# Performance work log

Hardware: AMD Instinct MI355X
Metric: run time of the kernel (lower is better)

## Reference

```python
import jax, jax.numpy as jnp
import numpy as np

B, V, N, H, C_OUT = 16, 8192, 2048, 128, 7


def setup_inputs() -> dict:
    key = jax.random.key(0)
    ks = jax.random.split(key, 5)
    return {
        "verts": jax.random.normal(ks[0], (B, V, 3), jnp.float32) * 10.0,
        "coords_ca": jax.random.normal(ks[1], (B, N, 3), jnp.float32) * 10.0,
        "feats": jax.random.normal(ks[2], (B, N, H), jnp.float32),
        "W1": jax.random.normal(ks[3], (H, H), jnp.float32) / np.sqrt(H),
        "b1": jnp.zeros((H,), jnp.float32),
        "W2": jax.random.normal(ks[4], (H, C_OUT), jnp.float32) / np.sqrt(H),
        "b2": jnp.zeros((C_OUT,), jnp.float32),
    }


def reference(verts, coords_ca, feats, W1, b1, W2, b2):
    # Per-graph: nearest-CA match for every surface vertex (cdist + argmin),
    # then sum over the UNIQUE set of matched residues (torch: processed[min_indices.unique()].sum(-2)).
    # Equivalent jit-friendly form: hit-mask over residues, masked sum.
    def per_graph(v, c, f):
        # squared euclidean distances [V, N]; argmin is invariant to the sqrt
        d = (jnp.sum(v * v, -1)[:, None]
             - 2.0 * (v @ c.T)
             + jnp.sum(c * c, -1)[None, :])
        mi = jnp.argmin(d, axis=1)                       # [V] nearest residue per vertex
        hit = jnp.zeros((c.shape[0],), f.dtype).at[mi].add(1.0)
        mask = (hit > 0).astype(f.dtype)                 # [N] residue selected at least once
        return jnp.einsum('nh,n->h', f, mask)            # sum over unique selected residues

    pooled = jax.vmap(per_graph)(verts, coords_ca, feats)  # [B, H]
    # top_net (Dropout is identity in eval)
    h = jax.nn.relu(pooled @ W1 + b1)
    return h @ W2 + b2                                    # [B, 7]
```

## Files before the change

kernel.cpp:

```cpp
#include <hip/hip_runtime.h>
#include <hip/hip_bf16.h>

#define B_GR   16
#define V_PTS  8192
#define N_RES  2048
#define H_DIM  128
#define C_OUT  7
#define SEGS   16

#define NSPLIT 16
#define NL     (N_RES / NSPLIT)
#define VPT    8
#define VBLK   (256 * VPT)
#define VBLKS  (V_PTS / VBLK)

__global__ __launch_bounds__(256, 4) void k_argmin(const float* __restrict__ verts,
                                                   const float* __restrict__ coords,
                                                   unsigned long long* __restrict__ mi64) {
    __shared__ float4 sc[NL];
    const int b  = blockIdx.x / (VBLKS * NSPLIT);
    const int r  = blockIdx.x % (VBLKS * NSPLIT);
    const int vb = r / NSPLIT;
    const int ns = r % NSPLIT;

    const float* cbase = coords + ((size_t)b * N_RES + ns * NL) * 3;
    if (threadIdx.x < NL) {
        const int i = threadIdx.x;
        float x = cbase[i * 3 + 0];
        float y = cbase[i * 3 + 1];
        float z = cbase[i * 3 + 2];
        float csq = __fadd_rn(__fadd_rn(__fmul_rn(x, x), __fmul_rn(y, y)), __fmul_rn(z, z));
        sc[i] = make_float4(x, y, z, csq);
    }
    __syncthreads();

    const int vbase = vb * VBLK + threadIdx.x;
    const float* vp = verts + (size_t)b * V_PTS * 3;

    float vx[VPT], vy[VPT], vz[VPT], vsq[VPT], best[VPT];
    int bi[VPT];
#pragma unroll
    for (int k = 0; k < VPT; ++k) {
        const int v = vbase + k * 256;
        vx[k] = vp[v * 3 + 0];
        vy[k] = vp[v * 3 + 1];
        vz[k] = vp[v * 3 + 2];
        vsq[k] = __fadd_rn(__fadd_rn(__fmul_rn(vx[k], vx[k]), __fmul_rn(vy[k], vy[k])),
                           __fmul_rn(vz[k], vz[k]));
        best[k] = 3.402823466e+38f;
        bi[k] = 0;
    }

#pragma unroll 2
    for (int n = 0; n < NL; ++n) {
        const float4 c = sc[n];
#pragma unroll
        for (int k = 0; k < VPT; ++k) {
            float dot = __fadd_rn(__fadd_rn(__fmul_rn(vx[k], c.x), __fmul_rn(vy[k], c.y)),
                                  __fmul_rn(vz[k], c.z));
            float d = __fadd_rn(fmaf(-2.0f, dot, vsq[k]), c.w);
            bool m = d < best[k];
            best[k] = m ? d : best[k];
            bi[k]   = m ? n : bi[k];
        }
    }

#pragma unroll
    for (int k = 0; k < VPT; ++k) {
        unsigned int bits = __float_as_uint(best[k]);
        unsigned int key  = bits ^ (unsigned int)(((int)bits >> 31) | 0x80000000);
        unsigned long long packed =
            ((unsigned long long)key << 32) | (unsigned int)(ns * NL + bi[k]);
        atomicMin(&mi64[(size_t)b * V_PTS + vbase + k * 256], packed);
    }
}

__global__ __launch_bounds__(256) void k_pool(const unsigned long long* __restrict__ mi64,
                                              const float* __restrict__ feats,
                                              float* __restrict__ partial) {
    __shared__ float msk[N_RES];
    __shared__ float4 red[8][32];
    const int b   = blockIdx.x >> 4;
    const int seg = blockIdx.x & (SEGS - 1);

    for (int i = threadIdx.x; i < N_RES; i += 256) msk[i] = 0.0f;
    __syncthreads();

    const unsigned long long* mb = mi64 + (size_t)b * V_PTS;
    for (int v = threadIdx.x; v < V_PTS; v += 256)
        msk[(unsigned int)mb[v]] = 1.0f;
    __syncthreads();

    const int q = threadIdx.x & 31;
    const int s = threadIdx.x >> 5;
    const int n0 = seg * (N_RES / SEGS);
    const float4* fb4 = (const float4*)(feats + ((size_t)b * N_RES + n0) * H_DIM);

    float4 acc = make_float4(0.f, 0.f, 0.f, 0.f);
#pragma unroll
    for (int n = 0; n < N_RES / SEGS / 8; ++n) {
        const int nn = s + n * 8;
        const float m = msk[n0 + nn];
        const float4 f = fb4[(size_t)nn * 32 + q];
        acc.x = fmaf(f.x, m, acc.x);
        acc.y = fmaf(f.y, m, acc.y);
        acc.z = fmaf(f.z, m, acc.z);
        acc.w = fmaf(f.w, m, acc.w);
    }
    red[s][q] = acc;
    __syncthreads();

    if (s == 0) {
        float4 t = acc;
#pragma unroll
        for (int i = 1; i < 8; ++i) {
            t.x += red[i][q].x; t.y += red[i][q].y;
            t.z += red[i][q].z; t.w += red[i][q].w;
        }
        ((float4*)partial)[((size_t)b * SEGS + seg) * 32 + q] = t;
    }
}

__global__ __launch_bounds__(128) void k_mlp(const float* __restrict__ partial,
                                             const float* __restrict__ W1,
                                             const float* __restrict__ b1,
                                             const float* __restrict__ W2,
                                             const float* __restrict__ b2,
                                             float* __restrict__ out) {
    __shared__ float pooled[H_DIM];
    __shared__ float h1[H_DIM];
    const int b = blockIdx.x;
    const int j = threadIdx.x;

    float s = 0.0f;
#pragma unroll
    for (int g = 0; g < SEGS; ++g)
        s += partial[((size_t)b * SEGS + g) * H_DIM + j];
    pooled[j] = s;
    __syncthreads();

    float acc = b1[j];
#pragma unroll 8
    for (int hh = 0; hh < H_DIM; ++hh)
        acc = fmaf(pooled[hh], W1[hh * H_DIM + j], acc);
    h1[j] = fmaxf(acc, 0.0f);
    __syncthreads();

    if (j < C_OUT) {
        float o = b2[j];
#pragma unroll 8
        for (int hh = 0; hh < H_DIM; ++hh)
            o = fmaf(h1[hh], W2[hh * C_OUT + j], o);
        out[(size_t)b * C_OUT + j] = o;
    }
}

extern "C" void kernel_launch(void* const* d_in, const int* in_sizes, int n_in,
                              void* d_out, int out_size, void* d_ws, size_t ws_size,
                              hipStream_t stream) {
    const float* verts  = (const float*)d_in[0];
    const float* coords = (const float*)d_in[1];
    const float* feats  = (const float*)d_in[2];
    const float* W1     = (const float*)d_in[3];
    const float* b1     = (const float*)d_in[4];
    const float* W2     = (const float*)d_in[5];
    const float* b2     = (const float*)d_in[6];
    float* out = (float*)d_out;

    unsigned long long* mi64 = (unsigned long long*)d_ws;
    float* partial = (float*)((char*)d_ws + (size_t)B_GR * V_PTS * 8);

    hipMemsetAsync(mi64, 0xFF, (size_t)B_GR * V_PTS * 8, stream);
    k_argmin<<<B_GR * VBLKS * NSPLIT, 256, 0, stream>>>(verts, coords, mi64);
    k_pool  <<<B_GR * SEGS,           256, 0, stream>>>(mi64, feats, partial);
    k_mlp   <<<B_GR,                  128, 0, stream>>>(partial, W1, b1, W2, b2, out);
}
```

Baseline: 150.0 us.

## Fuse memset, argmin, pool and MLP into one cooperative kernel with grid syncs

Replaces the memset plus three kernel launches with a single cooperative kernel that initializes the argmin buffer, computes nearest-residue argmin, builds masks, pools features and runs the MLP, with grid.sync between phases. The aim is to remove launch gaps and the separate memset. The residue split per block drops from 16 to 8, or 4 if the larger grid cannot be co-resident. That halves the grid (512 vs 1024 blocks) but doubles the work per block, and the grid syncs add barrier cost. The old path is kept as a fallback if the cooperative launch fails.

```diff
diff --git a/kernel.cpp b/kernel.cpp
--- a/kernel.cpp
+++ b/kernel.cpp
@@ -1,5 +1,8 @@
 #include <hip/hip_runtime.h>
 #include <hip/hip_bf16.h>
+#include <hip/hip_cooperative_groups.h>
+
+namespace cg = cooperative_groups;
 
 #define B_GR   16
 #define V_PTS  8192
@@ -8,23 +11,184 @@
 #define C_OUT  7
 #define SEGS   16
 
-#define NSPLIT 16
-#define NL     (N_RES / NSPLIT)
 #define VPT    8
 #define VBLK   (256 * VPT)
 #define VBLKS  (V_PTS / VBLK)
 
-__global__ __launch_bounds__(256, 4) void k_argmin(const float* __restrict__ verts,
-                                                   const float* __restrict__ coords,
-                                                   unsigned long long* __restrict__ mi64) {
-    __shared__ float4 sc[NL];
-    const int b  = blockIdx.x / (VBLKS * NSPLIT);
-    const int r  = blockIdx.x % (VBLKS * NSPLIT);
-    const int vb = r / NSPLIT;
-    const int ns = r % NSPLIT;
-
-    const float* cbase = coords + ((size_t)b * N_RES + ns * NL) * 3;
-    if (threadIdx.x < NL) {
+
+union ShMem {
+    float4 sc[N_RES / 4];
+    struct { float msk[N_RES]; float4 red[8][32]; } pool;
+    struct { float pooled[H_DIM]; float h1[H_DIM]; } mlp;
+};
+
+template <int NS>
+__global__ __launch_bounds__(256, 2) void k_fused(const float* __restrict__ verts,
+                                                  const float* __restrict__ coords,
+                                                  const float* __restrict__ feats,
+                                                  const float* __restrict__ W1,
+                                                  const float* __restrict__ b1,
+                                                  const float* __restrict__ W2,
+                                                  const float* __restrict__ b2,
+                                                  float* __restrict__ out,
+                                                  unsigned long long* __restrict__ mi64,
+                                                  float* __restrict__ partial) {
+    constexpr int NL = N_RES / NS;
+    cg::grid_group grid = cg::this_grid();
+    __shared__ ShMem u;
+
+    for (unsigned int gid = blockIdx.x * 256u + threadIdx.x;
+         gid < B_GR * V_PTS; gid += gridDim.x * 256u)
+        mi64[gid] = ~0ULL;
+    grid.sync();
+
+    {
+        const int b  = blockIdx.x / (VBLKS * NS);
+        const int r  = blockIdx.x % (VBLKS * NS);
+        const int vb = r / NS;
+        const int ns = r % NS;
+
+        const float* cbase = coords + ((size_t)b * N_RES + ns * NL) * 3;
+        for (int i = threadIdx.x; i < NL; i += 256) {
+            float x = cbase[i * 3 + 0];
+            float y = cbase[i * 3 + 1];
+            float z = cbase[i * 3 + 2];
+            float csq = __fadd_rn(__fadd_rn(__fmul_rn(x, x), __fmul_rn(y, y)), __fmul_rn(z, z));
+            u.sc[i] = make_float4(x, y, z, csq);
+        }
+        __syncthreads();
+
+        const int vbase = vb * VBLK + threadIdx.x;
+        const float* vp = verts + (size_t)b * V_PTS * 3;
+
+        float vx[VPT], vy[VPT], vz[VPT], vsq[VPT], best[VPT];
+        int bi[VPT];
+#pragma unroll
+        for (int k = 0; k < VPT; ++k) {
+            const int v = vbase + k * 256;
+            vx[k] = vp[v * 3 + 0];
+            vy[k] = vp[v * 3 + 1];
+            vz[k] = vp[v * 3 + 2];
+            vsq[k] = __fadd_rn(__fadd_rn(__fmul_rn(vx[k], vx[k]), __fmul_rn(vy[k], vy[k])),
+                               __fmul_rn(vz[k], vz[k]));
+            best[k] = 3.402823466e+38f;
+            bi[k] = 0;
+        }
+
+#pragma unroll 2
+        for (int n = 0; n < NL; ++n) {
+            const float4 c = u.sc[n];
+#pragma unroll
+            for (int k = 0; k < VPT; ++k) {
+                float dot = __fadd_rn(__fadd_rn(__fmul_rn(vx[k], c.x), __fmul_rn(vy[k], c.y)),
+                                      __fmul_rn(vz[k], c.z));
+                float d = __fadd_rn(fmaf(-2.0f, dot, vsq[k]), c.w);
+                bool m = d < best[k];
+                best[k] = m ? d : best[k];
+                bi[k]   = m ? n : bi[k];
+            }
+        }
+
+#pragma unroll
+        for (int k = 0; k < VPT; ++k) {
+            unsigned int bits = __float_as_uint(best[k]);
+            unsigned int key  = bits ^ (unsigned int)(((int)bits >> 31) | 0x80000000);
+            unsigned long long packed =
+                ((unsigned long long)key << 32) | (unsigned int)(ns * NL + bi[k]);
+            atomicMin(&mi64[(size_t)b * V_PTS + vbase + k * 256], packed);
+        }
+    }
+    grid.sync();
+
+    if (blockIdx.x < B_GR * SEGS) {
+        const int b   = blockIdx.x >> 4;
+        const int seg = blockIdx.x & (SEGS - 1);
+
+        for (int i = threadIdx.x; i < N_RES; i += 256) u.pool.msk[i] = 0.0f;
+        __syncthreads();
+
+        const unsigned long long* mb = mi64 + (size_t)b * V_PTS;
+        for (int v = threadIdx.x; v < V_PTS; v += 256)
+            u.pool.msk[(unsigned int)mb[v]] = 1.0f;
+        __syncthreads();
+
+        const int q = threadIdx.x & 31;
+        const int s = threadIdx.x >> 5;
+        const int n0 = seg * (N_RES / SEGS);
+        const float4* fb4 = (const float4*)(feats + ((size_t)b * N_RES + n0) * H_DIM);
+
+        float4 acc = make_float4(0.f, 0.f, 0.f, 0.f);
+#pragma unroll
+        for (int n = 0; n < N_RES / SEGS / 8; ++n) {
+            const int nn = s + n * 8;
+            const float m = u.pool.msk[n0 + nn];
+            const float4 f = fb4[(size_t)nn * 32 + q];
+            acc.x = fmaf(f.x, m, acc.x);
+            acc.y = fmaf(f.y, m, acc.y);
+            acc.z = fmaf(f.z, m, acc.z);
+            acc.w = fmaf(f.w, m, acc.w);
+        }
+        u.pool.red[s][q] = acc;
+        __syncthreads();
+
+        if (s == 0) {
+            float4 t = acc;
+#pragma unroll
+            for (int i = 1; i < 8; ++i) {
+                t.x += u.pool.red[i][q].x; t.y += u.pool.red[i][q].y;
+                t.z += u.pool.red[i][q].z; t.w += u.pool.red[i][q].w;
+            }
+            ((float4*)partial)[((size_t)b * SEGS + seg) * 32 + q] = t;
+        }
+    }
+    grid.sync();
+
+    if (blockIdx.x < B_GR) {
+        const int b = blockIdx.x;
+        const int j = threadIdx.x;
+
+        if (j < H_DIM) {
+            float s = 0.0f;
+#pragma unroll
+            for (int g = 0; g < SEGS; ++g)
+                s += partial[((size_t)b * SEGS + g) * H_DIM + j];
+            u.mlp.pooled[j] = s;
+        }
+        __syncthreads();
+
+        if (j < H_DIM) {
+            float acc = b1[j];
+#pragma unroll 8
+            for (int hh = 0; hh < H_DIM; ++hh)
+                acc = fmaf(u.mlp.pooled[hh], W1[hh * H_DIM + j], acc);
+            u.mlp.h1[j] = fmaxf(acc, 0.0f);
+        }
+        __syncthreads();
+
+        if (j < C_OUT) {
+            float o = b2[j];
+#pragma unroll 8
+            for (int hh = 0; hh < H_DIM; ++hh)
+                o = fmaf(u.mlp.h1[hh], W2[hh * C_OUT + j], o);
+            out[(size_t)b * C_OUT + j] = o;
+        }
+    }
+}
+
+#define FB_NSPLIT 16
+#define FB_NL     (N_RES / FB_NSPLIT)
+
+__global__ __launch_bounds__(256, 4) void k_argmin_fb(const float* __restrict__ verts,
+                                                      const float* __restrict__ coords,
+                                                      unsigned long long* __restrict__ mi64) {
+    __shared__ float4 sc[FB_NL];
+    const int b  = blockIdx.x / (VBLKS * FB_NSPLIT);
+    const int r  = blockIdx.x % (VBLKS * FB_NSPLIT);
+    const int vb = r / FB_NSPLIT;
+    const int ns = r % FB_NSPLIT;
+
+    const float* cbase = coords + ((size_t)b * N_RES + ns * FB_NL) * 3;
+    if (threadIdx.x < FB_NL) {
         const int i = threadIdx.x;
         float x = cbase[i * 3 + 0];
         float y = cbase[i * 3 + 1];
@@ -52,7 +216,7 @@
     }
 
 #pragma unroll 2
-    for (int n = 0; n < NL; ++n) {
+    for (int n = 0; n < FB_NL; ++n) {
         const float4 c = sc[n];
 #pragma unroll
         for (int k = 0; k < VPT; ++k) {
@@ -70,14 +234,14 @@
         unsigned int bits = __float_as_uint(best[k]);
         unsigned int key  = bits ^ (unsigned int)(((int)bits >> 31) | 0x80000000);
         unsigned long long packed =
-            ((unsigned long long)key << 32) | (unsigned int)(ns * NL + bi[k]);
+            ((unsigned long long)key << 32) | (unsigned int)(ns * FB_NL + bi[k]);
         atomicMin(&mi64[(size_t)b * V_PTS + vbase + k * 256], packed);
     }
 }
 
-__global__ __launch_bounds__(256) void k_pool(const unsigned long long* __restrict__ mi64,
-                                              const float* __restrict__ feats,
-                                              float* __restrict__ partial) {
+__global__ __launch_bounds__(256) void k_pool_fb(const unsigned long long* __restrict__ mi64,
+                                                 const float* __restrict__ feats,
+                                                 float* __restrict__ partial) {
     __shared__ float msk[N_RES];
     __shared__ float4 red[8][32];
     const int b   = blockIdx.x >> 4;
@@ -121,12 +285,12 @@
     }
 }
 
-__global__ __launch_bounds__(128) void k_mlp(const float* __restrict__ partial,
-                                             const float* __restrict__ W1,
-                                             const float* __restrict__ b1,
-                                             const float* __restrict__ W2,
-                                             const float* __restrict__ b2,
-                                             float* __restrict__ out) {
+__global__ __launch_bounds__(128) void k_mlp_fb(const float* __restrict__ partial,
+                                                const float* __restrict__ W1,
+                                                const float* __restrict__ b1,
+                                                const float* __restrict__ W2,
+                                                const float* __restrict__ b2,
+                                                float* __restrict__ out) {
     __shared__ float pooled[H_DIM];
     __shared__ float h1[H_DIM];
     const int b = blockIdx.x;
@@ -170,8 +334,24 @@
     unsigned long long* mi64 = (unsigned long long*)d_ws;
     float* partial = (float*)((char*)d_ws + (size_t)B_GR * V_PTS * 8);
 
-    hipMemsetAsync(mi64, 0xFF, (size_t)B_GR * V_PTS * 8, stream);
-    k_argmin<<<B_GR * VBLKS * NSPLIT, 256, 0, stream>>>(verts, coords, mi64);
-    k_pool  <<<B_GR * SEGS,           256, 0, stream>>>(mi64, feats, partial);
-    k_mlp   <<<B_GR,                  128, 0, stream>>>(partial, W1, b1, W2, b2, out);
-}
+    void* args[] = { (void*)&verts, (void*)&coords, (void*)&feats, (void*)&W1,
+                     (void*)&b1, (void*)&W2, (void*)&b2, (void*)&out,
+                     (void*)&mi64, (void*)&partial };
+
+    hipError_t e = hipLaunchCooperativeKernel((const void*)k_fused<8>,
+                                              dim3(B_GR * VBLKS * 8), dim3(256),
+                                              args, 0, stream);
+    if (e != hipSuccess) {
+        (void)hipGetLastError();
+        e = hipLaunchCooperativeKernel((const void*)k_fused<4>,
+                                       dim3(B_GR * VBLKS * 4), dim3(256),
+                                       args, 0, stream);
+    }
+    if (e != hipSuccess) {
+        (void)hipGetLastError();
+        hipMemsetAsync(mi64, 0xFF, (size_t)B_GR * V_PTS * 8, stream);
+        k_argmin_fb<<<B_GR * VBLKS * FB_NSPLIT, 256, 0, stream>>>(verts, coords, mi64);
+        k_pool_fb  <<<B_GR * SEGS,              256, 0, stream>>>(mi64, feats, partial);
+        k_mlp_fb   <<<B_GR,                     128, 0, stream>>>(partial, W1, b1, W2, b2, out);
+    }
+}
```

After: 286.8 us. +91.2%, slower.
